# Optimization experiments

Measured on AMD Instinct MI355X. Metric: run time of the kernel, lower is better.

## Reference

```python
import jax, jax.numpy as jnp
import numpy as np

N_QUBITS = 8
N_QLAYERS = 4
N_HEADS = 4
DIM = 2 ** N_QUBITS  # 256


def layer_norm(x, g, b, eps=1e-5):
    m = x.mean(-1, keepdims=True)
    v = ((x - m) ** 2).mean(-1, keepdims=True)
    return (x - m) / jnp.sqrt(v + eps) * g + b


def rx_mat(theta):
    # theta: scalar or [B]; returns [...,2,2] complex64
    h = theta * 0.5
    c = jnp.cos(h).astype(jnp.complex64)
    s = (jnp.sin(h) * (-1j)).astype(jnp.complex64)
    return jnp.stack([jnp.stack([c, s], -1), jnp.stack([s, c], -1)], -2)


def rz_mat(theta):
    h = (theta * 0.5).astype(jnp.complex64)
    e0 = jnp.exp(-1j * h)
    e1 = jnp.exp(1j * h)
    z = jnp.zeros_like(e0)
    return jnp.stack([jnp.stack([e0, z], -1), jnp.stack([z, e1], -1)], -2)


def apply_1q(state, U, wire, n):
    # state: [B, 2**n]; U: [2,2] (shared) or [B,2,2] (per-sample)
    B = state.shape[0]
    left = 2 ** wire
    right = 2 ** (n - 1 - wire)
    s = state.reshape(B, left, 2, right)
    if U.ndim == 2:
        s = jnp.einsum('jk,blkr->bljr', U, s)
    else:
        s = jnp.einsum('bjk,blkr->bljr', U, s)
    return s.reshape(B, 2 ** n)


def apply_cnot(state, ctrl, n):
    # CNOT with control=ctrl, target=ctrl+1 (adjacent wires)
    B = state.shape[0]
    left = 2 ** ctrl
    right = 2 ** (n - 2 - ctrl)
    s = state.reshape(B, left, 4, right)
    s = s[:, :, jnp.array([0, 1, 3, 2]), :]  # swap |10> and |11>
    return s.reshape(B, 2 ** n)


def quantum_expvals(angles, weights):
    # angles: [B, n_qubits] data-encoding angles; weights: [n_layers, 2, n_qubits]
    # Batched statevector sim of: RX(a_i)RZ(a_i) encoding, then per layer
    # RX(w[l,0,i]) RZ(w[l,1,i]) and a CNOT chain; returns <Z_i> per wire.
    n = N_QUBITS
    B = angles.shape[0]
    state = jnp.zeros((B, 2 ** n), jnp.complex64).at[:, 0].set(1.0)
    for i in range(n):
        state = apply_1q(state, rx_mat(angles[:, i]), i, n)
        state = apply_1q(state, rz_mat(angles[:, i]), i, n)
    for l in range(N_QLAYERS):
        for i in range(n):
            state = apply_1q(state, rx_mat(weights[l, 0, i]), i, n)
            state = apply_1q(state, rz_mat(weights[l, 1, i]), i, n)
        for i in range(n - 1):
            state = apply_cnot(state, i, n)
    probs = jnp.abs(state) ** 2  # [B, 2**n] float32
    zs = []
    for i in range(n):
        p = probs.reshape(B, 2 ** i, 2, 2 ** (n - 1 - i)).sum(axis=(1, 3))
        zs.append(p[:, 0] - p[:, 1])
    return jnp.stack(zs, -1)  # [B, n_qubits]


def mha(x, in_w, in_b, out_w, out_b):
    B, S, d = x.shape
    hd = d // N_HEADS
    qkv = x @ in_w.T + in_b  # [B,S,3d]
    q, k, v = jnp.split(qkv, 3, axis=-1)
    sp = lambda t: t.reshape(B, S, N_HEADS, hd).transpose(0, 2, 1, 3)
    q, k, v = sp(q), sp(k), sp(v)
    scores = jnp.einsum('bhqd,bhkd->bhqk', q, k) / np.sqrt(hd).astype(np.float32)
    attn = jax.nn.softmax(scores, axis=-1)
    o = jnp.einsum('bhqk,bhkd->bhqd', attn, v).transpose(0, 2, 1, 3).reshape(B, S, d)
    return o @ out_w.T + out_b


def _forward(x, attn_in_w, attn_in_b, attn_out_w, attn_out_b,
             ln1_g, ln1_b, ln2_g, ln2_b, ln3_g, ln3_b,
             qin_w, qin_b, qweights, qout_w, qout_b,
             ffn_w1, ffn_b1, ffn_w2, ffn_b2):
    attn_out = mha(x, attn_in_w, attn_in_b, attn_out_w, attn_out_b)
    x = layer_norm(x + attn_out, ln1_g, ln1_b)
    x_norm = layer_norm(x, ln3_g, ln3_b)
    B, S, d = x.shape
    flat = x_norm.reshape(B * S, d)
    angles = flat @ qin_w.T + qin_b  # [B*S, n_qubits]
    z = quantum_expvals(angles, qweights)
    q_out = (z @ qout_w.T + qout_b).reshape(B, S, d)
    x = x + q_out
    h = jax.nn.gelu(x @ ffn_w1.T + ffn_b1, approximate=False)  # torch GELU exact
    ffn_out = h @ ffn_w2.T + ffn_b2  # dropout is identity in eval
    return layer_norm(x + ffn_out, ln2_g, ln2_b)


def setup_inputs() -> dict:
    key = jax.random.key(0)
    ks = jax.random.split(key, 10)
    B, S, d, nq, nl = 32, 512, 512, N_QUBITS, N_QLAYERS
    rn = lambda k, sh, sc=0.02: jax.random.normal(k, sh, jnp.float32) * sc
    return {
        'x': jax.random.normal(ks[0], (B, S, d), jnp.float32),
        'attn_in_w': rn(ks[1], (3 * d, d)),
        'attn_in_b': jnp.zeros((3 * d,), jnp.float32),
        'attn_out_w': rn(ks[2], (d, d)),
        'attn_out_b': jnp.zeros((d,), jnp.float32),
        'ln1_g': jnp.ones((d,), jnp.float32), 'ln1_b': jnp.zeros((d,), jnp.float32),
        'ln2_g': jnp.ones((d,), jnp.float32), 'ln2_b': jnp.zeros((d,), jnp.float32),
        'ln3_g': jnp.ones((d,), jnp.float32), 'ln3_b': jnp.zeros((d,), jnp.float32),
        'qin_w': rn(ks[3], (nq, d), 0.05),
        'qin_b': jnp.zeros((nq,), jnp.float32),
        'qweights': jax.random.uniform(ks[4], (nl, 2, nq), jnp.float32, 0.0, 2.0 * np.pi),
        'qout_w': rn(ks[5], (d, nq), 0.1),
        'qout_b': jnp.zeros((d,), jnp.float32),
        'ffn_w1': rn(ks[6], (4 * d, d)),
        'ffn_b1': jnp.zeros((4 * d,), jnp.float32),
        'ffn_w2': rn(ks[7], (d, 4 * d)),
        'ffn_b2': jnp.zeros((d,), jnp.float32),
    }


def reference(x, attn_in_w, attn_in_b, attn_out_w, attn_out_b,
              ln1_g, ln1_b, ln2_g, ln2_b, ln3_g, ln3_b,
              qin_w, qin_b, qweights, qout_w, qout_b,
              ffn_w1, ffn_b1, ffn_w2, ffn_b2):
    return _forward(x, attn_in_w, attn_in_b, attn_out_w, attn_out_b,
                    ln1_g, ln1_b, ln2_g, ln2_b, ln3_g, ln3_b,
                    qin_w, qin_b, qweights, qout_w, qout_b,
                    ffn_w1, ffn_b1, ffn_w2, ffn_b2)
```

## Files before the change

kernel.cpp:

```cpp
#include <hip/hip_runtime.h>
#include <math.h>


typedef __bf16 bf16;
typedef bf16 bf16x8 __attribute__((ext_vector_type(8)));
typedef bf16 bf16x4 __attribute__((ext_vector_type(4)));
typedef float f32x4 __attribute__((ext_vector_type(4)));

__device__ __forceinline__ void gld16(const void* g, void* l) {
  __builtin_amdgcn_global_load_lds(
      (__attribute__((address_space(1))) void*)(void*)g,
      (__attribute__((address_space(3))) void*)l, 16, 0, 0);
}

__device__ __forceinline__ float waveAllSum(float v) {
#pragma unroll
  for (int m = 1; m < 64; m <<= 1) v += __shfl_xor(v, m, 64);
  return v;
}

__global__ __launch_bounds__(256) void cvt_all(
    const float* __restrict__ x, const float* __restrict__ w1,
    const float* __restrict__ w2, const float* __restrict__ w3,
    const float* __restrict__ w4, bf16* __restrict__ xb,
    bf16* __restrict__ b1, bf16* __restrict__ b2, bf16* __restrict__ b3,
    bf16* __restrict__ b4) {
  int i = blockIdx.x * 256 + threadIdx.x;
  const float* src;
  bf16* dst;
  int off;
  if (i < 2097152) {
    src = x; dst = xb; off = i;
  } else if (i < 2097152 + 196608) {
    src = w1; dst = b1; off = i - 2097152;
  } else if (i < 2097152 + 196608 + 65536) {
    src = w2; dst = b2; off = i - (2097152 + 196608);
  } else if (i < 2097152 + 196608 + 65536 + 262144) {
    src = w3; dst = b3; off = i - (2097152 + 196608 + 65536);
  } else {
    src = w4; dst = b4; off = i - (2097152 + 196608 + 65536 + 262144);
  }
  float4 v = ((const float4*)src)[off];
  bf16x4 o = {(bf16)v.x, (bf16)v.y, (bf16)v.z, (bf16)v.w};
  ((bf16x4*)dst)[off] = o;
}

__global__ void make_gates(const float* __restrict__ qw,
                           float* __restrict__ gates) {
  int t = threadIdx.x;
  if (t >= 32) return;
  int l = t >> 3, i = t & 7;
  float ax = qw[l * 16 + i] * 0.5f;
  float az = qw[l * 16 + 8 + i] * 0.5f;
  float cx, sx, cz, sz;
  sincosf(ax, &sx, &cx);
  sincosf(az, &sz, &cz);
  float* g = gates + t * 8;
  g[0] = cz * cx;   g[1] = -sz * cx;
  g[2] = -sz * sx;  g[3] = -cz * sx;
  g[4] = sz * sx;   g[5] = -cz * sx;
  g[6] = cz * cx;   g[7] = sz * cx;
}

__global__ __launch_bounds__(256) void gemm_mfma(
    const bf16* __restrict__ A, const bf16* __restrict__ W,
    const float* __restrict__ bias, float* __restrict__ Cf,
    bf16* __restrict__ Cb, bf16* __restrict__ qk, bf16* __restrict__ vT,
    int M, int N, int K, int mode) {
  __shared__ __align__(16) bf16 As[128 * 32];
  __shared__ __align__(16) bf16 Bs[128 * 32];
  int tid = threadIdx.x;
  int lane = tid & 63, w = tid >> 6;
  int wr = w >> 1, wc = w & 1;
  int quad = lane >> 4, lc = lane & 15;
  long m0 = (long)blockIdx.x * 128;
  long n0 = (long)blockIdx.y * 128;
  int r4 = lane >> 2;
  int koff = (lane & 3) * 8;
  f32x4 acc[4][4] = {};

  for (int k0 = 0; k0 < K; k0 += 32) {
    __syncthreads();
#pragma unroll
    for (int p = 0; p < 2; ++p) {
      int row = p * 64 + w * 16 + r4;
      gld16(A + (m0 + row) * (long)K + k0 + koff, &As[row * 32 + koff]);
      gld16(W + (n0 + row) * (long)K + k0 + koff, &Bs[row * 32 + koff]);
    }
    __syncthreads();
    bf16x8 af[4], bfr[4];
#pragma unroll
    for (int i = 0; i < 4; ++i) {
      af[i] = *(const bf16x8*)&As[(wr * 64 + i * 16 + lc) * 32 + quad * 8];
      bfr[i] = *(const bf16x8*)&Bs[(wc * 64 + i * 16 + lc) * 32 + quad * 8];
    }
#pragma unroll
    for (int i = 0; i < 4; ++i)
#pragma unroll
      for (int j = 0; j < 4; ++j)
        acc[i][j] = __builtin_amdgcn_mfma_f32_16x16x32_bf16(af[i], bfr[j],
                                                            acc[i][j], 0, 0, 0);
  }

#pragma unroll
  for (int i = 0; i < 4; ++i) {
    long grow0 = m0 + wr * 64 + i * 16 + quad * 4;
#pragma unroll
    for (int j = 0; j < 4; ++j) {
      long col = n0 + wc * 64 + j * 16 + lc;
      float bv = bias[col];
      float v[4];
#pragma unroll
      for (int r = 0; r < 4; ++r) v[r] = acc[i][j][r] + bv;
      if (mode == 0) {
#pragma unroll
        for (int r = 0; r < 4; ++r) Cf[(grow0 + r) * N + col] = v[r];
      } else if (mode == 1) {
#pragma unroll
        for (int r = 0; r < 4; ++r) {
          float g = 0.5f * v[r] * (1.0f + erff(v[r] * 0.70710678118654752f));
          Cb[(grow0 + r) * N + col] = (bf16)g;
        }
      } else {
        if (col < 1024) {
#pragma unroll
          for (int r = 0; r < 4; ++r) qk[(grow0 + r) * 1024 + col] = (bf16)v[r];
        } else {
          int hh = (int)((col - 1024) >> 7);
          int dd = (int)((col - 1024) & 127);
          long bidx = grow0 >> 9;
          int s0 = (int)(grow0 & 511);
          bf16x4 pk = {(bf16)v[0], (bf16)v[1], (bf16)v[2], (bf16)v[3]};
          *(bf16x4*)&vT[(((bidx << 2) + hh) * 128 + dd) * 512 + s0] = pk;
        }
      }
    }
  }
}

__global__ __launch_bounds__(256) void attn_mfma(const bf16* __restrict__ qk,
                                                 const bf16* __restrict__ vT,
                                                 bf16* __restrict__ o) {
  __shared__ __align__(16) bf16 Ks[64 * 128];
  __shared__ __align__(16) bf16 Vt[128 * 64];
  __shared__ __align__(16) bf16 Ps[4][64 * 16];
  int tid = threadIdx.x, lane = tid & 63, w = tid >> 6;
  int quad = lane >> 4, lc = lane & 15;
  int bh = blockIdx.x, b = bh >> 2, h = bh & 3;
  int q0 = blockIdx.y * 64 + w * 16;
  const float scale = 0.08838834764831845f;

  bf16x8 qf[4];
  {
    const bf16* qp =
        qk + ((long)(b * 512 + q0 + lc)) * 1024 + h * 128 + quad * 8;
#pragma unroll
    for (int ks = 0; ks < 4; ++ks) qf[ks] = *(const bf16x8*)(qp + ks * 32);
  }
  f32x4 oacc[8] = {};
  float mrun[4] = {-1e30f, -1e30f, -1e30f, -1e30f};
  float lrun[4] = {0.f, 0.f, 0.f, 0.f};

  const bf16* kbase = qk + (long)b * 512 * 1024 + 512 + h * 128;
  const bf16* vbase = vT + (long)bh * 128 * 512;
  int kr = lane >> 4, ke = (lane & 15) * 8;
  int vr = lane >> 3, ve = (lane & 7) * 8;

  for (int kt = 0; kt < 512; kt += 64) {
    __syncthreads();
#pragma unroll
    for (int c = 0; c < 4; ++c) {
      int row = w * 16 + c * 4 + kr;
      gld16(kbase + (long)(kt + row) * 1024 + ke, &Ks[row * 128 + ke]);
    }
#pragma unroll
    for (int c = 0; c < 4; ++c) {
      int row = w * 32 + c * 8 + vr;
      gld16(vbase + (long)row * 512 + kt + ve, &Vt[row * 64 + ve]);
    }
    __syncthreads();

    float p[4][4];
#pragma unroll
    for (int c = 0; c < 4; ++c) {
      f32x4 a = {};
#pragma unroll
      for (int ks = 0; ks < 4; ++ks) {
        bf16x8 kf = *(const bf16x8*)&Ks[(c * 16 + lc) * 128 + ks * 32 + quad * 8];
        a = __builtin_amdgcn_mfma_f32_16x16x32_bf16(qf[ks], kf, a, 0, 0, 0);
      }
#pragma unroll
      for (int r = 0; r < 4; ++r) p[c][r] = a[r] * scale;
    }

    float alpha[4];
#pragma unroll
    for (int r = 0; r < 4; ++r) {
      float mx = fmaxf(fmaxf(p[0][r], p[1][r]), fmaxf(p[2][r], p[3][r]));
#pragma unroll
      for (int m = 1; m < 16; m <<= 1) mx = fmaxf(mx, __shfl_xor(mx, m, 64));
      float mn = fmaxf(mrun[r], mx);
      alpha[r] = expf(mrun[r] - mn);
      mrun[r] = mn;
      float rs = 0.f;
#pragma unroll
      for (int c = 0; c < 4; ++c) {
        float e = expf(p[c][r] - mn);
        p[c][r] = e;
        rs += e;
      }
#pragma unroll
      for (int m = 1; m < 16; m <<= 1) rs += __shfl_xor(rs, m, 64);
      lrun[r] = lrun[r] * alpha[r] + rs;
    }
#pragma unroll
    for (int n = 0; n < 8; ++n)
#pragma unroll
      for (int r = 0; r < 4; ++r) oacc[n][r] *= alpha[r];

#pragma unroll
    for (int c = 0; c < 4; ++c) {
      bf16x4 pk = {(bf16)p[c][0], (bf16)p[c][1], (bf16)p[c][2], (bf16)p[c][3]};
      *(bf16x4*)&Ps[w][(c * 16 + lc) * 16 + quad * 4] = pk;
    }
    bf16x8 pf[2];
#pragma unroll
    for (int kc = 0; kc < 2; ++kc) {
      bf16x8 t;
#pragma unroll
      for (int jj = 0; jj < 8; ++jj)
        t[jj] = Ps[w][(kc * 32 + quad * 8 + jj) * 16 + lc];
      pf[kc] = t;
    }
#pragma unroll
    for (int n = 0; n < 8; ++n)
#pragma unroll
      for (int kc = 0; kc < 2; ++kc) {
        bf16x8 vf = *(const bf16x8*)&Vt[(n * 16 + lc) * 64 + kc * 32 + quad * 8];
        oacc[n] =
            __builtin_amdgcn_mfma_f32_16x16x32_bf16(pf[kc], vf, oacc[n], 0, 0, 0);
      }
  }

  float linv[4];
#pragma unroll
  for (int r = 0; r < 4; ++r) linv[r] = 1.0f / lrun[r];
  bf16* op = o + ((long)(b * 512 + q0 + quad * 4)) * 512 + h * 128 + lc;
#pragma unroll
  for (int n = 0; n < 8; ++n)
#pragma unroll
    for (int r = 0; r < 4; ++r)
      op[(long)r * 512 + n * 16] = (bf16)(oacc[n][r] * linv[r]);
}

__global__ __launch_bounds__(256) void add_ln_kernel(
    const float* __restrict__ a, const float* __restrict__ b,
    const float* __restrict__ g, const float* __restrict__ be,
    float* __restrict__ out) {
  long row = (blockIdx.x * 256 + threadIdx.x) >> 6;
  int lane = threadIdx.x & 63;
  const float* ar = a + row * 512;
  const float* br = b + row * 512;
  float v[8];
  float s = 0.f;
#pragma unroll
  for (int j = 0; j < 8; ++j) {
    int c = lane + 64 * j;
    v[j] = ar[c] + br[c];
    s += v[j];
  }
  s = waveAllSum(s);
  float mean = s * (1.0f / 512.0f);
  float var = 0.f;
#pragma unroll
  for (int j = 0; j < 8; ++j) {
    float d = v[j] - mean;
    var = fmaf(d, d, var);
  }
  var = waveAllSum(var);
  float rstd = rsqrtf(var * (1.0f / 512.0f) + 1e-5f);
  float* orow = out + row * 512;
#pragma unroll
  for (int j = 0; j < 8; ++j) {
    int c = lane + 64 * j;
    orow[c] = (v[j] - mean) * rstd * g[c] + be[c];
  }
}

__global__ __launch_bounds__(256) void quantum_kernel(
    const float* __restrict__ x, const float* __restrict__ attnp,
    const float* __restrict__ g1, const float* __restrict__ b1,
    const float* __restrict__ g3, const float* __restrict__ b3,
    const float* __restrict__ qin_w, const float* __restrict__ qin_b,
    const float* __restrict__ gates, const float* __restrict__ qout_w,
    const float* __restrict__ qout_b, float* __restrict__ x2,
    bf16* __restrict__ x2b) {
  long row = (blockIdx.x * 256 + threadIdx.x) >> 6;
  int lane = threadIdx.x & 63;
  const float* xr = x + row * 512;
  const float* ar = attnp + row * 512;

  float x1v[8];
  {
    float s = 0.f;
#pragma unroll
    for (int j = 0; j < 8; ++j) {
      int c = lane + 64 * j;
      x1v[j] = xr[c] + ar[c];
      s += x1v[j];
    }
    s = waveAllSum(s);
    float mean = s * (1.0f / 512.0f);
    float var = 0.f;
#pragma unroll
    for (int j = 0; j < 8; ++j) {
      float d = x1v[j] - mean;
      var = fmaf(d, d, var);
    }
    var = waveAllSum(var);
    float rstd = rsqrtf(var * (1.0f / 512.0f) + 1e-5f);
#pragma unroll
    for (int j = 0; j < 8; ++j) {
      int c = lane + 64 * j;
      x1v[j] = (x1v[j] - mean) * rstd * g1[c] + b1[c];
    }
  }

  float xn[8];
  {
    float s = 0.f;
#pragma unroll
    for (int j = 0; j < 8; ++j) s += x1v[j];
    s = waveAllSum(s);
    float mean = s * (1.0f / 512.0f);
    float var = 0.f;
#pragma unroll
    for (int j = 0; j < 8; ++j) {
      float d = x1v[j] - mean;
      var = fmaf(d, d, var);
    }
    var = waveAllSum(var);
    float rstd = rsqrtf(var * (1.0f / 512.0f) + 1e-5f);
#pragma unroll
    for (int j = 0; j < 8; ++j) {
      int c = lane + 64 * j;
      xn[j] = (x1v[j] - mean) * rstd * g3[c] + b3[c];
    }
  }

  float ang[8];
#pragma unroll
  for (int w = 0; w < 8; ++w) {
    float p = 0.f;
#pragma unroll
    for (int j = 0; j < 8; ++j)
      p = fmaf(xn[j], qin_w[w * 512 + lane + 64 * j], p);
    p = waveAllSum(p);
    ang[w] = p + qin_b[w];
  }

  float sr[4], si[4];
  sr[0] = (lane == 0) ? 1.0f : 0.0f;
  sr[1] = sr[2] = sr[3] = 0.0f;
  si[0] = si[1] = si[2] = si[3] = 0.0f;

  auto gate = [&](int p, float u00r, float u00i, float u01r, float u01i,
                  float u10r, float u10i, float u11r, float u11i) {
    if (p >= 2) {
      int m = 1 << (p - 2);
      int b = (lane >> (p - 2)) & 1;
      float csr = b ? u11r : u00r;
      float csi = b ? u11i : u00i;
      float cor = b ? u10r : u01r;
      float coi = b ? u10i : u01i;
#pragma unroll
      for (int l = 0; l < 4; ++l) {
        float pr = __shfl_xor(sr[l], m, 64);
        float pi = __shfl_xor(si[l], m, 64);
        float nr = fmaf(csr, sr[l],
                        fmaf(-csi, si[l], fmaf(cor, pr, -coi * pi)));
        float ni = fmaf(csr, si[l],
                        fmaf(csi, sr[l], fmaf(cor, pi, coi * pr)));
        sr[l] = nr;
        si[l] = ni;
      }
    } else {
      float nr[4], ni[4];
#pragma unroll
      for (int l = 0; l < 4; ++l) {
        int b = (l >> p) & 1;
        int pl = l ^ (1 << p);
        float csr = b ? u11r : u00r;
        float csi = b ? u11i : u00i;
        float cor = b ? u10r : u01r;
        float coi = b ? u10i : u01i;
        nr[l] = fmaf(csr, sr[l],
                     fmaf(-csi, si[l], fmaf(cor, sr[pl], -coi * si[pl])));
        ni[l] = fmaf(csr, si[l],
                     fmaf(csi, sr[l], fmaf(cor, si[pl], coi * sr[pl])));
      }
#pragma unroll
      for (int l = 0; l < 4; ++l) {
        sr[l] = nr[l];
        si[l] = ni[l];
      }
    }
  };

  auto docnot = [&](int i) {
    int pc = 7 - i, pt = 6 - i;
    if (pt >= 2) {
      int ctrl = (lane >> (pc - 2)) & 1;
      int m = 1 << (pt - 2);
#pragma unroll
      for (int l = 0; l < 4; ++l) {
        float pr = __shfl_xor(sr[l], m, 64);
        float pi = __shfl_xor(si[l], m, 64);
        if (ctrl) {
          sr[l] = pr;
          si[l] = pi;
        }
      }
    } else if (pt == 1) {
      if (lane & 1) {
        float t;
        t = sr[0]; sr[0] = sr[2]; sr[2] = t;
        t = si[0]; si[0] = si[2]; si[2] = t;
        t = sr[1]; sr[1] = sr[3]; sr[3] = t;
        t = si[1]; si[1] = si[3]; si[3] = t;
      }
    } else {
      float t;
      t = sr[2]; sr[2] = sr[3]; sr[3] = t;
      t = si[2]; si[2] = si[3]; si[3] = t;
    }
  };

#pragma unroll
  for (int i = 0; i < 8; ++i) {
    float half = ang[i] * 0.5f;
    float c, s;
    sincosf(half, &s, &c);
    float cc = c * c, sc = s * c, ss = s * s;
    gate(7 - i, cc, -sc, -ss, -sc, ss, -sc, cc, sc);
  }
#pragma unroll
  for (int l = 0; l < 4; ++l) {
#pragma unroll
    for (int i = 0; i < 8; ++i) {
      const float* g = gates + (l * 8 + i) * 8;
      gate(7 - i, g[0], g[1], g[2], g[3], g[4], g[5], g[6], g[7]);
    }
#pragma unroll
    for (int i = 0; i < 7; ++i) docnot(i);
  }

  float pr4[4];
#pragma unroll
  for (int l = 0; l < 4; ++l) pr4[l] = sr[l] * sr[l] + si[l] * si[l];
  float z[8];
#pragma unroll
  for (int w = 0; w < 8; ++w) {
    int p = 7 - w;
    float part = 0.f;
#pragma unroll
    for (int l = 0; l < 4; ++l) {
      int bit = (p >= 2) ? ((lane >> (p - 2)) & 1) : ((l >> p) & 1);
      part += bit ? -pr4[l] : pr4[l];
    }
    z[w] = waveAllSum(part);
  }

  float* orow = x2 + row * 512;
  bf16* brow = x2b + row * 512;
#pragma unroll
  for (int j = 0; j < 8; ++j) {
    int col = lane + 64 * j;
    float acc = qout_b[col];
#pragma unroll
    for (int w = 0; w < 8; ++w) acc = fmaf(z[w], qout_w[col * 8 + w], acc);
    float val = x1v[j] + acc;
    orow[col] = val;
    brow[col] = (bf16)val;
  }
}

extern "C" void kernel_launch(void* const* d_in, const int* in_sizes, int n_in,
                              void* d_out, int out_size, void* d_ws,
                              size_t ws_size, hipStream_t stream) {
  const float* x = (const float*)d_in[0];
  const float* attn_in_w = (const float*)d_in[1];
  const float* attn_in_b = (const float*)d_in[2];
  const float* attn_out_w = (const float*)d_in[3];
  const float* attn_out_b = (const float*)d_in[4];
  const float* ln1_g = (const float*)d_in[5];
  const float* ln1_b = (const float*)d_in[6];
  const float* ln2_g = (const float*)d_in[7];
  const float* ln2_b = (const float*)d_in[8];
  const float* ln3_g = (const float*)d_in[9];
  const float* ln3_b = (const float*)d_in[10];
  const float* qin_w = (const float*)d_in[11];
  const float* qin_b = (const float*)d_in[12];
  const float* qweights = (const float*)d_in[13];
  const float* qout_w = (const float*)d_in[14];
  const float* qout_b = (const float*)d_in[15];
  const float* ffn_w1 = (const float*)d_in[16];
  const float* ffn_b1 = (const float*)d_in[17];
  const float* ffn_w2 = (const float*)d_in[18];
  const float* ffn_b2 = (const float*)d_in[19];

  char* wsB = (char*)d_ws;
  bf16* qkb = (bf16*)(wsB);
  bf16* vtb = (bf16*)(wsB + (32L << 20));
  bf16* ob = (bf16*)(wsB + (48L << 20));
  bf16* hb = (bf16*)(wsB);
  float* slot1 = (float*)(wsB + (64L << 20));
  float* x2 = (float*)(wsB + (96L << 20));
  bf16* x2b = (bf16*)(wsB + (128L << 20));
  bf16* xb = (bf16*)(wsB + (144L << 20));
  bf16* w_in = (bf16*)(wsB + (160L << 20));
  bf16* w_out = (bf16*)(wsB + (162L << 20));
  bf16* w_f1 = (bf16*)(wsB + (163L << 20));
  bf16* w_f2 = (bf16*)(wsB + (165L << 20));
  float* gates = (float*)(wsB + (167L << 20));

  const int M = 16384;
  float* outp = (float*)d_out;

  cvt_all<<<11264, 256, 0, stream>>>(x, attn_in_w, attn_out_w, ffn_w1, ffn_w2,
                                     xb, w_in, w_out, w_f1, w_f2);
  make_gates<<<1, 64, 0, stream>>>(qweights, gates);

  gemm_mfma<<<dim3(M / 128, 12), 256, 0, stream>>>(
      xb, w_in, attn_in_b, nullptr, nullptr, qkb, vtb, M, 1536, 512, 2);
  attn_mfma<<<dim3(128, 8), 256, 0, stream>>>(qkb, vtb, ob);
  gemm_mfma<<<dim3(M / 128, 4), 256, 0, stream>>>(
      ob, w_out, attn_out_b, slot1, nullptr, nullptr, nullptr, M, 512, 512, 0);
  quantum_kernel<<<dim3(M / 4), 256, 0, stream>>>(
      x, slot1, ln1_g, ln1_b, ln3_g, ln3_b, qin_w, qin_b, gates, qout_w,
      qout_b, x2, x2b);
  gemm_mfma<<<dim3(M / 128, 16), 256, 0, stream>>>(
      x2b, w_f1, ffn_b1, nullptr, hb, nullptr, nullptr, M, 2048, 512, 1);
  gemm_mfma<<<dim3(M / 128, 4), 256, 0, stream>>>(
      hb, w_f2, ffn_b2, slot1, nullptr, nullptr, nullptr, M, 512, 2048, 0);
  add_ln_kernel<<<dim3(M / 4), 256, 0, stream>>>(x2, slot1, ln2_g, ln2_b,
                                                 outp);
}
```

Measured before the change: 503.5 us.

## Recast quantum circuit as a fixed unitary applied by MFMA GEMM

The weight-only part of the circuit (variational layers plus CNOT chains) is folded once into a 256x256 complex unitary, stored as a 512x512 real bf16 matrix. Each token's encoded product state is built in closed form and multiplied by that matrix on the MFMA GEMM. The Z expectation values and qout projection are fused into a second GEMM with a ±1 sign matrix, and the residual add happens in its epilogue. This replaces the per-token shuffle-heavy statevector simulation with tensor-core work, at the cost of extra launches, intermediate traffic, and bf16 rounding of amplitudes and probabilities.

```diff
diff --git a/kernel.cpp b/kernel.cpp
--- a/kernel.cpp
+++ b/kernel.cpp
@@ -62,11 +62,125 @@
   g[6] = cz * cx;   g[7] = sz * cx;
 }
 
+__global__ __launch_bounds__(256) void make_W(const float* __restrict__ gates,
+                                              bf16* __restrict__ Wp) {
+  int tid = threadIdx.x, lane = tid & 63;
+  int k = blockIdx.x * 4 + (tid >> 6);
+
+  float sr[4], si[4];
+#pragma unroll
+  for (int l = 0; l < 4; ++l) {
+    sr[l] = (lane * 4 + l == k) ? 1.0f : 0.0f;
+    si[l] = 0.0f;
+  }
+
+  auto gate = [&](int p, float u00r, float u00i, float u01r, float u01i,
+                  float u10r, float u10i, float u11r, float u11i) {
+    if (p >= 2) {
+      int m = 1 << (p - 2);
+      int b = (lane >> (p - 2)) & 1;
+      float csr = b ? u11r : u00r;
+      float csi = b ? u11i : u00i;
+      float cor = b ? u10r : u01r;
+      float coi = b ? u10i : u01i;
+#pragma unroll
+      for (int l = 0; l < 4; ++l) {
+        float pr = __shfl_xor(sr[l], m, 64);
+        float pi = __shfl_xor(si[l], m, 64);
+        float nr = fmaf(csr, sr[l],
+                        fmaf(-csi, si[l], fmaf(cor, pr, -coi * pi)));
+        float ni = fmaf(csr, si[l],
+                        fmaf(csi, sr[l], fmaf(cor, pi, coi * pr)));
+        sr[l] = nr;
+        si[l] = ni;
+      }
+    } else {
+      float nr[4], ni[4];
+#pragma unroll
+      for (int l = 0; l < 4; ++l) {
+        int b = (l >> p) & 1;
+        int pl = l ^ (1 << p);
+        float csr = b ? u11r : u00r;
+        float csi = b ? u11i : u00i;
+        float cor = b ? u10r : u01r;
+        float coi = b ? u10i : u01i;
+        nr[l] = fmaf(csr, sr[l],
+                     fmaf(-csi, si[l], fmaf(cor, sr[pl], -coi * si[pl])));
+        ni[l] = fmaf(csr, si[l],
+                     fmaf(csi, sr[l], fmaf(cor, si[pl], coi * sr[pl])));
+      }
+#pragma unroll
+      for (int l = 0; l < 4; ++l) {
+        sr[l] = nr[l];
+        si[l] = ni[l];
+      }
+    }
+  };
+  auto docnot = [&](int i) {
+    int pc = 7 - i, pt = 6 - i;
+    if (pt >= 2) {
+      int ctrl = (lane >> (pc - 2)) & 1;
+      int m = 1 << (pt - 2);
+#pragma unroll
+      for (int l = 0; l < 4; ++l) {
+        float pr = __shfl_xor(sr[l], m, 64);
+        float pi = __shfl_xor(si[l], m, 64);
+        if (ctrl) {
+          sr[l] = pr;
+          si[l] = pi;
+        }
+      }
+    } else if (pt == 1) {
+      if (lane & 1) {
+        float t;
+        t = sr[0]; sr[0] = sr[2]; sr[2] = t;
+        t = si[0]; si[0] = si[2]; si[2] = t;
+        t = sr[1]; sr[1] = sr[3]; sr[3] = t;
+        t = si[1]; si[1] = si[3]; si[3] = t;
+      }
+    } else {
+      float t;
+      t = sr[2]; sr[2] = sr[3]; sr[3] = t;
+      t = si[2]; si[2] = si[3]; si[3] = t;
+    }
+  };
+
+  for (int l = 0; l < 4; ++l) {
+    for (int i = 0; i < 8; ++i) {
+      const float* g = gates + (l * 8 + i) * 8;
+      gate(7 - i, g[0], g[1], g[2], g[3], g[4], g[5], g[6], g[7]);
+    }
+    for (int i = 0; i < 7; ++i) docnot(i);
+  }
+
+#pragma unroll
+  for (int l = 0; l < 4; ++l) {
+    int j = lane * 4 + l;
+    Wp[j * 512 + k] = (bf16)sr[l];
+    Wp[j * 512 + 256 + k] = (bf16)(-si[l]);
+    Wp[(j + 256) * 512 + k] = (bf16)si[l];
+    Wp[(j + 256) * 512 + 256 + k] = (bf16)sr[l];
+  }
+}
+
+__global__ __launch_bounds__(256) void make_Q(const float* __restrict__ qout_w,
+                                              bf16* __restrict__ Q) {
+  int t = blockIdx.x * 256 + threadIdx.x;
+  int col = t >> 8, k = t & 255;
+  float s = 0.f;
+#pragma unroll
+  for (int w = 0; w < 8; ++w) {
+    float sg = ((k >> (7 - w)) & 1) ? -1.0f : 1.0f;
+    s = fmaf(qout_w[col * 8 + w], sg, s);
+  }
+  Q[col * 256 + k] = (bf16)s;
+}
+
 __global__ __launch_bounds__(256) void gemm_mfma(
     const bf16* __restrict__ A, const bf16* __restrict__ W,
-    const float* __restrict__ bias, float* __restrict__ Cf,
-    bf16* __restrict__ Cb, bf16* __restrict__ qk, bf16* __restrict__ vT,
-    int M, int N, int K, int mode) {
+    const float* __restrict__ bias, const float* __restrict__ Xadd,
+    float* __restrict__ Cf, bf16* __restrict__ Cb, bf16* __restrict__ qk,
+    bf16* __restrict__ vT, int M, int N, int K, int mode) {
   __shared__ __align__(16) bf16 As[128 * 32];
   __shared__ __align__(16) bf16 Bs[128 * 32];
   int tid = threadIdx.x;
@@ -108,7 +222,7 @@
 #pragma unroll
     for (int j = 0; j < 4; ++j) {
       long col = n0 + wc * 64 + j * 16 + lc;
-      float bv = bias[col];
+      float bv = (mode == 3) ? 0.f : bias[col];
       float v[4];
 #pragma unroll
       for (int r = 0; r < 4; ++r) v[r] = acc[i][j][r] + bv;
@@ -120,6 +234,16 @@
         for (int r = 0; r < 4; ++r) {
           float g = 0.5f * v[r] * (1.0f + erff(v[r] * 0.70710678118654752f));
           Cb[(grow0 + r) * N + col] = (bf16)g;
+        }
+      } else if (mode == 3) {
+#pragma unroll
+        for (int r = 0; r < 4; ++r) Cb[(grow0 + r) * N + col] = (bf16)v[r];
+      } else if (mode == 4) {
+#pragma unroll
+        for (int r = 0; r < 4; ++r) {
+          float val = v[r] + Xadd[(grow0 + r) * N + col];
+          Cf[(grow0 + r) * N + col] = val;
+          Cb[(grow0 + r) * N + col] = (bf16)val;
         }
       } else {
         if (col < 1024) {
@@ -287,14 +411,12 @@
   }
 }
 
-__global__ __launch_bounds__(256) void quantum_kernel(
+__global__ __launch_bounds__(256) void quantum_pre(
     const float* __restrict__ x, const float* __restrict__ attnp,
     const float* __restrict__ g1, const float* __restrict__ b1,
     const float* __restrict__ g3, const float* __restrict__ b3,
     const float* __restrict__ qin_w, const float* __restrict__ qin_b,
-    const float* __restrict__ gates, const float* __restrict__ qout_w,
-    const float* __restrict__ qout_b, float* __restrict__ x2,
-    bf16* __restrict__ x2b) {
+    float* __restrict__ x1out, bf16* __restrict__ psi) {
   long row = (blockIdx.x * 256 + threadIdx.x) >> 6;
   int lane = threadIdx.x & 63;
   const float* xr = x + row * 512;
@@ -325,6 +447,9 @@
       x1v[j] = (x1v[j] - mean) * rstd * g1[c] + b1[c];
     }
   }
+  float* x1row = x1out + row * 512;
+#pragma unroll
+  for (int j = 0; j < 8; ++j) x1row[lane + 64 * j] = x1v[j];
 
   float xn[8];
   {
@@ -359,130 +484,67 @@
     ang[w] = p + qin_b[w];
   }
 
-  float sr[4], si[4];
-  sr[0] = (lane == 0) ? 1.0f : 0.0f;
-  sr[1] = sr[2] = sr[3] = 0.0f;
-  si[0] = si[1] = si[2] = si[3] = 0.0f;
-
-  auto gate = [&](int p, float u00r, float u00i, float u01r, float u01i,
-                  float u10r, float u10i, float u11r, float u11i) {
-    if (p >= 2) {
-      int m = 1 << (p - 2);
-      int b = (lane >> (p - 2)) & 1;
-      float csr = b ? u11r : u00r;
-      float csi = b ? u11i : u00i;
-      float cor = b ? u10r : u01r;
-      float coi = b ? u10i : u01i;
-#pragma unroll
-      for (int l = 0; l < 4; ++l) {
-        float pr = __shfl_xor(sr[l], m, 64);
-        float pi = __shfl_xor(si[l], m, 64);
-        float nr = fmaf(csr, sr[l],
-                        fmaf(-csi, si[l], fmaf(cor, pr, -coi * pi)));
-        float ni = fmaf(csr, si[l],
-                        fmaf(csi, sr[l], fmaf(cor, pi, coi * pr)));
-        sr[l] = nr;
-        si[l] = ni;
-      }
-    } else {
-      float nr[4], ni[4];
-#pragma unroll
-      for (int l = 0; l < 4; ++l) {
-        int b = (l >> p) & 1;
-        int pl = l ^ (1 << p);
-        float csr = b ? u11r : u00r;
-        float csi = b ? u11i : u00i;
-        float cor = b ? u10r : u01r;
-        float coi = b ? u10i : u01i;
-        nr[l] = fmaf(csr, sr[l],
-                     fmaf(-csi, si[l], fmaf(cor, sr[pl], -coi * si[pl])));
-        ni[l] = fmaf(csr, si[l],
-                     fmaf(csi, sr[l], fmaf(cor, si[pl], coi * sr[pl])));
-      }
-#pragma unroll
-      for (int l = 0; l < 4; ++l) {
-        sr[l] = nr[l];
-        si[l] = ni[l];
-      }
-    }
-  };
-
-  auto docnot = [&](int i) {
-    int pc = 7 - i, pt = 6 - i;
-    if (pt >= 2) {
-      int ctrl = (lane >> (pc - 2)) & 1;
-      int m = 1 << (pt - 2);
-#pragma unroll
-      for (int l = 0; l < 4; ++l) {
-        float pr = __shfl_xor(sr[l], m, 64);
-        float pi = __shfl_xor(si[l], m, 64);
-        if (ctrl) {
-          sr[l] = pr;
-          si[l] = pi;
-        }
-      }
-    } else if (pt == 1) {
-      if (lane & 1) {
-        float t;
-        t = sr[0]; sr[0] = sr[2]; sr[2] = t;
-        t = si[0]; si[0] = si[2]; si[2] = t;
-        t = sr[1]; sr[1] = sr[3]; sr[3] = t;
-        t = si[1]; si[1] = si[3]; si[3] = t;
-      }
-    } else {
-      float t;
-      t = sr[2]; sr[2] = sr[3]; sr[3] = t;
-      t = si[2]; si[2] = si[3]; si[3] = t;
-    }
-  };
-
+  float v0r[8], v0i[8], v1r[8];
 #pragma unroll
   for (int i = 0; i < 8; ++i) {
-    float half = ang[i] * 0.5f;
+    float h = ang[i] * 0.5f;
     float c, s;
-    sincosf(half, &s, &c);
-    float cc = c * c, sc = s * c, ss = s * s;
-    gate(7 - i, cc, -sc, -ss, -sc, ss, -sc, cc, sc);
-  }
+    sincosf(h, &s, &c);
+    v0r[i] = c * c;
+    v0i[i] = -c * s;
+    v1r[i] = s * s;
+  }
+
+  float Pr, Pi;
+  {
+    int bit0 = (lane >> 5) & 1;
+    Pr = bit0 ? v1r[0] : v0r[0];
+    Pi = v0i[0];
+#pragma unroll
+    for (int i = 1; i < 6; ++i) {
+      int bit = (lane >> (5 - i)) & 1;
+      float br = bit ? v1r[i] : v0r[i];
+      float bi = v0i[i];
+      float nr = Pr * br - Pi * bi;
+      float ni = Pr * bi + Pi * br;
+      Pr = nr;
+      Pi = ni;
+    }
+  }
+
+  bf16 rebuf[4], imbuf[4];
 #pragma unroll
   for (int l = 0; l < 4; ++l) {
-#pragma unroll
-    for (int i = 0; i < 8; ++i) {
-      const float* g = gates + (l * 8 + i) * 8;
-      gate(7 - i, g[0], g[1], g[2], g[3], g[4], g[5], g[6], g[7]);
-    }
-#pragma unroll
-    for (int i = 0; i < 7; ++i) docnot(i);
-  }
-
-  float pr4[4];
-#pragma unroll
-  for (int l = 0; l < 4; ++l) pr4[l] = sr[l] * sr[l] + si[l] * si[l];
-  float z[8];
-#pragma unroll
-  for (int w = 0; w < 8; ++w) {
-    int p = 7 - w;
-    float part = 0.f;
-#pragma unroll
-    for (int l = 0; l < 4; ++l) {
-      int bit = (p >= 2) ? ((lane >> (p - 2)) & 1) : ((l >> p) & 1);
-      part += bit ? -pr4[l] : pr4[l];
-    }
-    z[w] = waveAllSum(part);
-  }
-
-  float* orow = x2 + row * 512;
-  bf16* brow = x2b + row * 512;
-#pragma unroll
-  for (int j = 0; j < 8; ++j) {
-    int col = lane + 64 * j;
-    float acc = qout_b[col];
-#pragma unroll
-    for (int w = 0; w < 8; ++w) acc = fmaf(z[w], qout_w[col * 8 + w], acc);
-    float val = x1v[j] + acc;
-    orow[col] = val;
-    brow[col] = (bf16)val;
-  }
+    int b6 = (l >> 1) & 1, b7 = l & 1;
+    float br = b6 ? v1r[6] : v0r[6], bi = v0i[6];
+    float tr = Pr * br - Pi * bi;
+    float ti = Pr * bi + Pi * br;
+    float cr = b7 ? v1r[7] : v0r[7], ci = v0i[7];
+    float fr = tr * cr - ti * ci;
+    float fi = tr * ci + ti * cr;
+    rebuf[l] = (bf16)fr;
+    imbuf[l] = (bf16)fi;
+  }
+  bf16* prow = psi + row * 512;
+  *(bf16x4*)&prow[lane * 4] = *(bf16x4*)rebuf;
+  *(bf16x4*)&prow[256 + lane * 4] = *(bf16x4*)imbuf;
+}
+
+__global__ __launch_bounds__(256) void prob_kernel(const bf16* __restrict__ phi,
+                                                   bf16* __restrict__ prob) {
+  int t4 = blockIdx.x * 256 + threadIdx.x;
+  int token = t4 >> 6;
+  int k4 = (t4 & 63) * 4;
+  const bf16* pr = phi + (long)token * 512;
+  bf16x4 re = *(const bf16x4*)&pr[k4];
+  bf16x4 im = *(const bf16x4*)&pr[256 + k4];
+  bf16 ob[4];
+#pragma unroll
+  for (int l = 0; l < 4; ++l) {
+    float r = (float)re[l], i = (float)im[l];
+    ob[l] = (bf16)(r * r + i * i);
+  }
+  *(bf16x4*)&prob[(long)token * 256 + k4] = *(bf16x4*)ob;
 }
 
 extern "C" void kernel_launch(void* const* d_in, const int* in_sizes, int n_in,
@@ -515,14 +577,21 @@
   bf16* ob = (bf16*)(wsB + (48L << 20));
   bf16* hb = (bf16*)(wsB);
   float* slot1 = (float*)(wsB + (64L << 20));
-  float* x2 = (float*)(wsB + (96L << 20));
-  bf16* x2b = (bf16*)(wsB + (128L << 20));
-  bf16* xb = (bf16*)(wsB + (144L << 20));
-  bf16* w_in = (bf16*)(wsB + (160L << 20));
-  bf16* w_out = (bf16*)(wsB + (162L << 20));
-  bf16* w_f1 = (bf16*)(wsB + (163L << 20));
-  bf16* w_f2 = (bf16*)(wsB + (165L << 20));
-  float* gates = (float*)(wsB + (167L << 20));
+  bf16* phi = (bf16*)(wsB + (64L << 20));
+  bf16* probb = (bf16*)(wsB + (80L << 20));
+  float* f2out = (float*)(wsB + (64L << 20));
+  float* x1 = (float*)(wsB + (96L << 20));
+  float* x2 = (float*)(wsB + (128L << 20));
+  bf16* x2b = (bf16*)(wsB + (160L << 20));
+  bf16* xb = (bf16*)(wsB + (176L << 20));
+  bf16* psi = (bf16*)(wsB + (176L << 20));
+  bf16* w_in = (bf16*)(wsB + (192L << 20));
+  bf16* w_out = (bf16*)(wsB + (194L << 20));
+  bf16* w_f1 = (bf16*)(wsB + (195L << 20));
+  bf16* w_f2 = (bf16*)(wsB + (197L << 20));
+  float* gates = (float*)(wsB + (199L << 20));
+  bf16* Wp = (bf16*)(wsB + (200L << 20));
+  bf16* Qm = (bf16*)(wsB + (201L << 20));
 
   const int M = 16384;
   float* outp = (float*)d_out;
@@ -530,19 +599,30 @@
   cvt_all<<<11264, 256, 0, stream>>>(x, attn_in_w, attn_out_w, ffn_w1, ffn_w2,
                                      xb, w_in, w_out, w_f1, w_f2);
   make_gates<<<1, 64, 0, stream>>>(qweights, gates);
+  make_W<<<64, 256, 0, stream>>>(gates, Wp);
+  make_Q<<<512, 256, 0, stream>>>(qout_w, Qm);
 
   gemm_mfma<<<dim3(M / 128, 12), 256, 0, stream>>>(
-      xb, w_in, attn_in_b, nullptr, nullptr, qkb, vtb, M, 1536, 512, 2);
+      xb, w_in, attn_in_b, nullptr, nullptr, nullptr, qkb, vtb, M, 1536, 512,
+      2);
   attn_mfma<<<dim3(128, 8), 256, 0, stream>>>(qkb, vtb, ob);
   gemm_mfma<<<dim3(M / 128, 4), 256, 0, stream>>>(
-      ob, w_out, attn_out_b, slot1, nullptr, nullptr, nullptr, M, 512, 512, 0);
-  quantum_kernel<<<dim3(M / 4), 256, 0, stream>>>(
-      x, slot1, ln1_g, ln1_b, ln3_g, ln3_b, qin_w, qin_b, gates, qout_w,
-      qout_b, x2, x2b);
+      ob, w_out, attn_out_b, nullptr, slot1, nullptr, nullptr, nullptr, M, 512,
+      512, 0);
+  quantum_pre<<<dim3(M / 4), 256, 0, stream>>>(x, slot1, ln1_g, ln1_b, ln3_g,
+                                               ln3_b, qin_w, qin_b, x1, psi);
+  gemm_mfma<<<dim3(M / 128, 4), 256, 0, stream>>>(
+      psi, Wp, nullptr, nullptr, nullptr, phi, nullptr, nullptr, M, 512, 512,
+      3);
+  prob_kernel<<<4096, 256, 0, stream>>>(phi, probb);
+  gemm_mfma<<<dim3(M / 128, 4), 256, 0, stream>>>(
+      probb, Qm, qout_b, x1, x2, x2b, nullptr, nullptr, M, 512, 256, 4);
   gemm_mfma<<<dim3(M / 128, 16), 256, 0, stream>>>(
-      x2b, w_f1, ffn_b1, nullptr, hb, nullptr, nullptr, M, 2048, 512, 1);
+      x2b, w_f1, ffn_b1, nullptr, nullptr, hb, nullptr, nullptr, M, 2048, 512,
+      1);
   gemm_mfma<<<dim3(M / 128, 4), 256, 0, stream>>>(
-      hb, w_f2, ffn_b2, slot1, nullptr, nullptr, nullptr, M, 512, 2048, 0);
-  add_ln_kernel<<<dim3(M / 4), 256, 0, stream>>>(x2, slot1, ln2_g, ln2_b,
+      hb, w_f2, ffn_b2, nullptr, f2out, nullptr, nullptr, nullptr, M, 512,
+      2048, 0);
+  add_ln_kernel<<<dim3(M / 4), 256, 0, stream>>>(x2, f2out, ln2_g, ln2_b,
                                                  outp);
 }
```

Result: slower. 518.5 us (+3.0%).
